# Kernel tuning notes

Hardware: AMD Instinct MI355X
Metric: run time of the kernel (lower is better)

Reference implementation:

```python
import jax, jax.numpy as jnp
from jax import lax
import numpy as np

BATCH, SEQ_LEN, ENC_IN, C_OUT = 16, 512, 32, 32
N_ORDER = 256           # window_size
MULTISCALE = (1, 2, 4)
MODES = min(32, SEQ_LEN // 2)  # = 32


def make_hippo(N, dt):
    """HiPPO-LegT transition, bilinear (Tustin) discretization, Legendre eval matrix."""
    Q = np.arange(N, dtype=np.float64)
    R = (2 * Q + 1)[:, None]
    j, i = np.meshgrid(Q, Q)
    A = np.where(i < j, -1.0, (-1.0) ** (i - j + 1)) * R
    B = (-1.0) ** Q[:, None] * R                      # [N,1]
    I = np.eye(N)
    M = I - (dt / 2.0) * A
    Ad = np.linalg.solve(M, I + (dt / 2.0) * A)
    Bd = np.linalg.solve(M, dt * B).squeeze(-1)       # [N]
    vals = np.arange(0.0, 1.0, dt)
    x = 1.0 - 2.0 * vals
    P = np.zeros((N, len(vals)))
    P[0] = 1.0
    if N > 1:
        P[1] = x
    for n in range(1, N - 1):
        P[n + 1] = ((2 * n + 1) * x * P[n] - n * P[n - 1]) / (n + 1)
    E = P.T                                           # [len(vals), N]
    return Ad.astype(np.float32), Bd.astype(np.float32), E.astype(np.float32)


def setup_inputs():
    key = jax.random.key(0)
    ks = jax.random.split(key, 12)
    inp = {}
    inp['x_enc'] = jax.random.normal(ks[0], (BATCH, SEQ_LEN, ENC_IN), jnp.float32)
    inp['x_mark_enc'] = jax.random.normal(ks[1], (BATCH, SEQ_LEN, 4), jnp.float32)
    inp['x_dec'] = jax.random.normal(ks[2], (BATCH, SEQ_LEN, ENC_IN), jnp.float32)
    inp['x_mark_dec'] = jax.random.normal(ks[3], (BATCH, SEQ_LEN, 4), jnp.float32)
    inp['affine_weight'] = jnp.ones((1, 1, ENC_IN), jnp.float32)
    inp['affine_bias'] = jnp.zeros((1, 1, ENC_IN), jnp.float32)
    scale = 1.0 / (N_ORDER * N_ORDER)
    for s in range(3):
        inp[f'wr{s}'] = scale * jax.random.uniform(ks[4 + 2 * s], (N_ORDER, N_ORDER, MODES), jnp.float32)
        inp[f'wi{s}'] = scale * jax.random.uniform(ks[5 + 2 * s], (N_ORDER, N_ORDER, MODES), jnp.float32)
    inp['mlp_w'] = 0.1 * jax.random.normal(ks[10], (1, 3), jnp.float32)
    inp['mlp_b'] = jnp.zeros((1,), jnp.float32)
    inp['proj_w'] = 0.02 * jax.random.normal(ks[11], (ENC_IN, C_OUT), jnp.float32)
    inp['proj_b'] = jnp.zeros((C_OUT,), jnp.float32)
    for s, m in enumerate(MULTISCALE):
        A, Bv, E = make_hippo(N_ORDER, 1.0 / SEQ_LEN / m)
        inp[f'A{s}'] = jnp.asarray(A)
        inp[f'Bv{s}'] = jnp.asarray(Bv)
        inp[f'E{s}'] = jnp.asarray(E)
    return inp


def _hippo_scan(x, A, Bv):
    # x: [B, L, C] -> cs: [L, B, C, N]; c_t = A c_{t-1} + B f_t (applied on last dim)
    B_, L, C = x.shape
    c0 = jnp.zeros((B_, C, A.shape[0]), x.dtype)
    At = A.T
    def step(c, f):                      # f: [B, C]
        c = c @ At + f[..., None] * Bv
        return c, c
    _, cs = lax.scan(step, c0, jnp.transpose(x, (1, 0, 2)))
    return cs


def _spectral_conv(xc, wr, wi):
    # xc: [B, C, N, L]; keep first MODES rfft bins, complex channel mix over N, irfft
    L = xc.shape[-1]
    xf = jnp.fft.rfft(xc)                                # [B,C,N,L//2+1] complex64
    W = (wr + 1j * wi).astype(jnp.complex64)             # [N,N,MODES]
    out = jnp.einsum('bjix,iox->bjox', xf[..., :MODES], W)
    out_ft = jnp.pad(out, ((0, 0), (0, 0), (0, 0), (0, L // 2 + 1 - MODES)))
    return jnp.fft.irfft(out_ft, n=L)                    # [B,C,N,L]


def _forward(x_enc, affine_weight, affine_bias, specs, mlp_w, mlp_b, proj_w, proj_b, hippos):
    means = lax.stop_gradient(jnp.mean(x_enc, axis=1, keepdims=True))
    xc = x_enc - means
    stdev = lax.stop_gradient(jnp.sqrt(jnp.var(xc, axis=1, keepdims=True) + 1e-5))
    x = xc / stdev
    x = x * affine_weight + affine_bias                  # [B, L, C]
    pred_len = SEQ_LEN
    decs = []
    for (wr, wi), (A, Bv, E) in zip(specs, hippos):
        # multiscale slice x[:, -m*pred_len:] clips to full seq_len since pred_len==seq_len
        cs = _hippo_scan(x, A, Bv)                       # [L,B,C,N]
        x_in_c = jnp.transpose(cs, (1, 2, 3, 0))         # [B,C,N,L]
        out1 = _spectral_conv(x_in_c, wr, wi)            # [B,C,N,L]
        x_dec_c = out1[..., pred_len - 1]                # [B,C,N]
        dec = x_dec_c @ E[-pred_len:, :].T               # [B,C,pred_len]
        decs.append(dec)
    stacked = jnp.stack(decs, axis=-1)                   # [B,C,P,3]
    y = stacked @ mlp_w[0] + mlp_b[0]                    # Linear(3,1) + squeeze -> [B,C,P]
    y = jnp.transpose(y, (0, 2, 1))                      # [B,P,C]
    y = (y - affine_bias) / (affine_weight + 1e-10)
    y = y * stdev + means
    return y @ proj_w + proj_b                           # OutputBlock: per-step channel projection


def reference(x_enc, x_mark_enc, x_dec, x_mark_dec, affine_weight, affine_bias,
              wr0, wi0, wr1, wi1, wr2, wi2, mlp_w, mlp_b, proj_w, proj_b,
              A0, Bv0, E0, A1, Bv1, E1, A2, Bv2, E2):
    specs = [(wr0, wi0), (wr1, wi1), (wr2, wi2)]
    hippos = [(A0, Bv0, E0), (A1, Bv1, E1), (A2, Bv2, E2)]
    return _forward(x_enc, affine_weight, affine_bias, specs, mlp_w, mlp_b, proj_w, proj_b, hippos)
```

## Files before the change

### kernel.cpp

```cpp
#include <hip/hip_runtime.h>
#include <math.h>

#define SEQ 512
#define NORD 256
#define MODES 32
#define KBIG (NORD*MODES*2)
#define PI_F 3.14159265358979323846f

typedef _Float16 half8 __attribute__((ext_vector_type(8)));
typedef float floatx4 __attribute__((ext_vector_type(4)));


struct GJob {
  const float* A; const float* B; float* C; const float* scale_ptr;
  int M, N, lda, k0, k1, atomic;
};
struct GJobs { GJob j[6]; };

__global__ __launch_bounds__(256) void gemm32_k(GJobs P) {
  GJob jb = P.j[blockIdx.z];
  int col0 = blockIdx.x * 32;
  int row0 = blockIdx.y * 32;
  if (row0 >= jb.M || col0 >= jb.N) return;
  __shared__ float As[64][34];
  __shared__ float Bs[64][36];
  int tid = threadIdx.x;
  int tx = tid & 15, ty = tid >> 4;
  const float* A = jb.A; const float* B = jb.B;
  int M = jb.M, N = jb.N, lda = jb.lda;
  int kcA = (tid & 15) * 4, rA = tid >> 4;
  int ccB = (tid & 7) * 4, kkB = tid >> 3;
  int gr0 = row0 + rA, gr1 = row0 + rA + 16;
  const float4 z4 = make_float4(0.f, 0.f, 0.f, 0.f);
  float4 a0, a1, b0, b1;
  {
    int kb = jb.k0;
    a0 = (gr0 < M) ? *(const float4*)&A[(size_t)gr0 * lda + kb + kcA] : z4;
    a1 = (gr1 < M) ? *(const float4*)&A[(size_t)gr1 * lda + kb + kcA] : z4;
    b0 = *(const float4*)&B[(size_t)(kb + kkB) * N + col0 + ccB];
    b1 = *(const float4*)&B[(size_t)(kb + kkB + 32) * N + col0 + ccB];
  }
  float acc00 = 0.f, acc01 = 0.f, acc10 = 0.f, acc11 = 0.f;
  for (int kb = jb.k0; kb < jb.k1; kb += 64) {
    As[kcA+0][rA] = a0.x; As[kcA+1][rA] = a0.y; As[kcA+2][rA] = a0.z; As[kcA+3][rA] = a0.w;
    As[kcA+0][rA+16] = a1.x; As[kcA+1][rA+16] = a1.y; As[kcA+2][rA+16] = a1.z; As[kcA+3][rA+16] = a1.w;
    *(float4*)&Bs[kkB][ccB] = b0;
    *(float4*)&Bs[kkB+32][ccB] = b1;
    __syncthreads();
    if (kb + 64 < jb.k1) {
      int kn = kb + 64;
      a0 = (gr0 < M) ? *(const float4*)&A[(size_t)gr0 * lda + kn + kcA] : z4;
      a1 = (gr1 < M) ? *(const float4*)&A[(size_t)gr1 * lda + kn + kcA] : z4;
      b0 = *(const float4*)&B[(size_t)(kn + kkB) * N + col0 + ccB];
      b1 = *(const float4*)&B[(size_t)(kn + kkB + 32) * N + col0 + ccB];
    }
    #pragma unroll
    for (int k = 0; k < 64; k++) {
      float2 av = *(float2*)&As[k][ty * 2];
      float2 bv = *(float2*)&Bs[k][tx * 2];
      acc00 += av.x * bv.x; acc01 += av.x * bv.y;
      acc10 += av.y * bv.x; acc11 += av.y * bv.y;
    }
    __syncthreads();
  }
  float sc = jb.scale_ptr ? *jb.scale_ptr : 1.f;
  int gr = row0 + ty * 2, gc = col0 + tx * 2;
  float v00 = acc00 * sc, v01 = acc01 * sc, v10 = acc10 * sc, v11 = acc11 * sc;
  if (jb.atomic) {
    if (gr < M)     { atomicAdd(&jb.C[(size_t)gr * N + gc], v00);     atomicAdd(&jb.C[(size_t)gr * N + gc + 1], v01); }
    if (gr + 1 < M) { atomicAdd(&jb.C[(size_t)(gr+1) * N + gc], v10); atomicAdd(&jb.C[(size_t)(gr+1) * N + gc + 1], v11); }
  } else {
    if (gr < M)     { jb.C[(size_t)gr * N + gc] = v00;     jb.C[(size_t)gr * N + gc + 1] = v01; }
    if (gr + 1 < M) { jb.C[(size_t)(gr+1) * N + gc] = v10; jb.C[(size_t)(gr+1) * N + gc + 1] = v11; }
  }
}


__global__ __launch_bounds__(256) void prep_k(const float* A0, const float* A1, const float* A2,
                                              const float* B0, const float* B1, const float* B2,
                                              const float* E0, const float* E1, const float* E2,
                                              float* R, float* Kry, float* Et, float* Z) {
  long bid = blockIdx.x;
  if (bid < 768) {
    long idx = bid * 256 + threadIdx.x;
    int scl = (int)(idx >> 16);
    int r = (int)(idx & 65535);
    int m = r >> 8, i2 = r & 255;
    const float* A = scl == 0 ? A0 : (scl == 1 ? A1 : A2);
    R[(size_t)scl * 2 * 65536 + (size_t)m * 256 + i2] = A[(size_t)i2 * 256 + m];
  } else if (bid < 2304) {
    long idx = (bid - 768) * 256 + threadIdx.x;
    int scl = (int)(idx / 131072);
    int r = (int)(idx % 131072);
    int p = r >> 8, o = r & 255;
    const float* E; int rows;
    if (scl == 0) { E = E0; rows = 512; }
    else if (scl == 1) { E = E1; rows = 1024; }
    else { E = E2; rows = 2048; }
    int base = rows - 512;
    Et[(size_t)scl * 131072 + (size_t)o * 512 + p] = E[(size_t)(base + p) * 256 + o];
  } else if (bid < 2307) {
    int scl = (int)(bid - 2304);
    const float* B = scl == 0 ? B0 : (scl == 1 ? B1 : B2);
    Kry[(size_t)scl * 512 * 256 + threadIdx.x] = B[threadIdx.x];
  } else {
    long idx = (bid - 2307) * 256 + threadIdx.x;
    if (idx < 655360) Z[idx] = 0.f;
  }
}


__global__ __launch_bounds__(256) void revin_k(const float* __restrict__ x,
                                               const float* __restrict__ aw,
                                               const float* __restrict__ ab,
                                               float* __restrict__ F,
                                               float* __restrict__ stats) {
  int row = blockIdx.x;
  int b = row >> 5, c = row & 31;
  int tid = threadIdx.x;
  const float* xp = x + (size_t)b * SEQ * 32 + c;
  float v0 = xp[(size_t)tid * 32];
  float v1 = xp[(size_t)(tid + 256) * 32];
  float s = v0 + v1, s2 = v0 * v0 + v1 * v1;
  for (int off = 32; off; off >>= 1) {
    s  += __shfl_down(s,  off, 64);
    s2 += __shfl_down(s2, off, 64);
  }
  __shared__ float ws1[4], ws2[4];
  __shared__ float mean_s, istd_s;
  int wid = tid >> 6, lane = tid & 63;
  if (lane == 0) { ws1[wid] = s; ws2[wid] = s2; }
  __syncthreads();
  if (tid == 0) {
    float t1 = ws1[0] + ws1[1] + ws1[2] + ws1[3];
    float t2 = ws2[0] + ws2[1] + ws2[2] + ws2[3];
    float mean = t1 / 512.f;
    float var = t2 / 512.f - mean * mean;
    float sd = sqrtf(var + 1e-5f);
    mean_s = mean; istd_s = 1.f / sd;
    stats[row] = mean; stats[512 + row] = sd;
  }
  __syncthreads();
  float w = aw[c], bb = ab[c];
  float m = mean_s, is = istd_s;
  F[(size_t)row * SEQ + tid]       = (v0 - m) * is * w + bb;
  F[(size_t)row * SEQ + tid + 256] = (v1 - m) * is * w + bb;
}


__global__ __launch_bounds__(256) void qbuildA_k(const float* __restrict__ Kry,
                                                 float2* __restrict__ Pp, int s0) {
  int bg = blockIdx.x;
  int s = s0 + (bg >> 8);
  int r = bg & 255;
  int k = r & 31, c = r >> 5;
  const float* Kry_s = Kry + (size_t)s * 131072;
  float2* P = Pp + (size_t)s * 65536;
  int i = threadIdx.x;
  float ar = 0.f, ai = 0.f;
  const float step = 2.f * PI_F / 512.f;
  int m0 = c * 64;
  for (int mm = 0; mm < 64; mm++) {
    int m = m0 + mm;
    float kap = Kry_s[(size_t)m * 256 + i];
    float sn, cn; __sincosf(step * (float)((k * m) & 511), &sn, &cn);
    ar += kap * cn; ai -= kap * sn;
  }
  P[(size_t)(c * 32 + k) * 256 + i] = make_float2(ar, ai);
}

__global__ __launch_bounds__(256) void qbuildB_k(const float* __restrict__ Kry,
                                                 const float2* __restrict__ Pp,
                                                 _Float16* __restrict__ Qf, int s0) {
  int bg = blockIdx.x;
  int slab = bg >> 8;
  int s = s0 + slab;
  int r = bg & 255;
  int ig = r & 31, c = r >> 5;
  const float* Kry_s = Kry + (size_t)s * 131072;
  const float2* P = Pp + (size_t)s * 65536;
  unsigned int* Qd = (unsigned int*)(Qf + (size_t)slab * 8388608);
  int tid = threadIdx.x;
  int k = tid & 31, il = tid >> 5;
  int i = ig * 8 + il;
  __shared__ __align__(16) unsigned int buf[16 * 256];
  float ar = 0.f, ai = 0.f;
  for (int cp = 0; cp < c; cp++) {
    float2 p = P[(size_t)(cp * 32 + k) * 256 + i];
    ar += p.x; ai += p.y;
  }
  const float step = 2.f * PI_F / 512.f;
  int m0 = c * 64;
  for (int mb = 0; mb < 64; mb += 16) {
    #pragma unroll
    for (int mm = 0; mm < 16; mm++) {
      int m = m0 + mb + mm;
      float kap = Kry_s[(size_t)m * 256 + i];
      float sn, cn; __sincosf(step * (float)((k * m) & 511), &sn, &cn);
      ar += kap * cn; ai -= kap * sn;
      int st = 511 - m;
      float sn2, cn2; __sincosf(step * (float)((k * st) & 511), &sn2, &cn2);
      float qr = ar * cn2 + ai * sn2;
      float qi = ai * cn2 - ar * sn2;
      qr = fminf(fmaxf(qr, -60000.f), 60000.f);
      qi = fminf(fmaxf(qi, -60000.f), 60000.f);
      _Float16 h0 = (_Float16)qr, h1 = (_Float16)qi;
      unsigned short u0, u1;
      __builtin_memcpy(&u0, &h0, 2); __builtin_memcpy(&u1, &h1, 2);
      buf[(st & 15) * 256 + il * 32 + k] = (unsigned int)u0 | ((unsigned int)u1 << 16);
    }
    __syncthreads();
    int st_hi = 511 - (m0 + mb);
    #pragma unroll
    for (int p = 0; p < 4; p++) {
      int idx = p * 256 + tid;
      int rr = idx >> 6, part = idx & 63;
      int st = st_hi - 15 + rr;
      uint4 v = *(uint4*)&buf[(st & 15) * 256 + part * 4];
      *(uint4*)&Qd[(size_t)st * 8192 + (size_t)ig * 256 + part * 4] = v;
    }
    __syncthreads();
  }
}


__global__ __launch_bounds__(256) void wbigT_k(const float* wr0, const float* wi0,
                                               const float* wr1, const float* wi1,
                                               const float* wr2, const float* wi2,
                                               _Float16* __restrict__ Wt, int s0) {
  int bg = blockIdx.x;
  int slab = bg >> 8;
  int s = s0 + slab;
  int r = bg & 255;
  int og = r & 31, iq = r >> 5;
  const float* wr = s == 0 ? wr0 : (s == 1 ? wr1 : wr2);
  const float* wi = s == 0 ? wi0 : (s == 1 ? wi1 : wi2);
  unsigned int* Wd = (unsigned int*)(Wt + (size_t)slab * 4194304);
  int tid = threadIdx.x;
  int ol = tid >> 5, k = tid & 31;
  int o = og * 8 + ol;
  float sn, cn; __sincosf((2.f * PI_F / 512.f) * (float)k, &sn, &cn);
  float g = ((k == 0) ? (1.f / 512.f) : (2.f / 512.f)) * 4096.f;
  float gc = g * cn, gs = g * sn;
  for (int ii = 0; ii < 32; ii++) {
    int i = iq * 32 + ii;
    float a = wr[(size_t)i * 8192 + o * 32 + k];
    float b = wi[(size_t)i * 8192 + o * 32 + k];
    float v0 = gc * a + gs * b;
    float v1 = gs * a - gc * b;
    _Float16 h0 = (_Float16)v0, h1 = (_Float16)v1;
    unsigned short u0, u1;
    __builtin_memcpy(&u0, &h0, 2); __builtin_memcpy(&u1, &h1, 2);
    Wd[(size_t)o * 8192 + (size_t)i * 32 + k] = (unsigned int)u0 | ((unsigned int)u1 << 16);
  }
}


__global__ __launch_bounds__(256) void umfma_k(const _Float16* __restrict__ Qf,
                                               const _Float16* __restrict__ Wt,
                                               float* __restrict__ U, int s0) {
  __shared__ __align__(16) _Float16 Al[8192];
  __shared__ __align__(16) _Float16 Bl[8192];
  int slab = blockIdx.z >> 4;
  int kslab = blockIdx.z & 15;
  int s = s0 + slab;
  const _Float16* Q = Qf + (size_t)slab * 8388608;
  const _Float16* W = Wt + (size_t)slab * 4194304;
  float* Us = U + (size_t)s * 131072;
  int m0 = blockIdx.x * 128;
  int n0 = blockIdx.y * 128;
  int kb0 = kslab * 1024;
  int tid = threadIdx.x;
  int w = tid >> 6, lane = tid & 63;
  int quad = lane >> 4, lm = lane & 15;
  floatx4 acc[4][4];
  #pragma unroll
  for (int a = 0; a < 4; a++)
    #pragma unroll
    for (int b = 0; b < 4; b++) acc[a][b] = (floatx4)(0.f);
  int wm = (w & 1) * 64, wn = (w >> 1) * 64;
  for (int kb = kb0; kb < kb0 + 1024; kb += 64) {
    __syncthreads();
    #pragma unroll
    for (int p = 0; p < 4; p++) {
      int idx = p * 256 + tid;
      int row = idx >> 3, kc = idx & 7;
      int slot = ((kc >> 2) * 8 + (row >> 4)) * 64 + (kc & 3) * 16 + (row & 15);
      *(half8*)&Al[slot * 8] = *(const half8*)&Q[(size_t)(m0 + row) * 16384 + kb + kc * 8];
      *(half8*)&Bl[slot * 8] = *(const half8*)&W[(size_t)(n0 + row) * 16384 + kb + kc * 8];
    }
    __syncthreads();
    #pragma unroll
    for (int ks = 0; ks < 2; ks++) {
      half8 af[4], bf[4];
      #pragma unroll
      for (int t = 0; t < 4; t++) {
        int mt = (wm >> 4) + t;
        af[t] = *(half8*)&Al[((ks * 8 + mt) * 64 + quad * 16 + lm) * 8];
        int nt = (wn >> 4) + t;
        bf[t] = *(half8*)&Bl[((ks * 8 + nt) * 64 + quad * 16 + lm) * 8];
      }
      #pragma unroll
      for (int mi = 0; mi < 4; mi++)
        #pragma unroll
        for (int ni = 0; ni < 4; ni++)
          acc[mi][ni] = __builtin_amdgcn_mfma_f32_16x16x32_f16(af[mi], bf[ni], acc[mi][ni], 0, 0, 0);
    }
  }
  #pragma unroll
  for (int mi = 0; mi < 4; mi++) {
    int gr0 = m0 + wm + mi * 16 + quad * 4;
    #pragma unroll
    for (int ni = 0; ni < 4; ni++) {
      int gc = n0 + wn + ni * 16 + lm;
      #pragma unroll
      for (int r = 0; r < 4; r++)
        atomicAdd(&Us[(size_t)(gr0 + r) * 256 + gc], acc[mi][ni][r] * (1.f / 4096.f));
    }
  }
}


__global__ __launch_bounds__(256) void final_k(const float* __restrict__ y0,
                                               const float* __restrict__ stats,
                                               const float* __restrict__ aw,
                                               const float* __restrict__ ab,
                                               const float* __restrict__ mlp_b,
                                               const float* __restrict__ pw,
                                               const float* __restrict__ pb,
                                               float* __restrict__ out) {
  int b = blockIdx.y;
  int p0 = blockIdx.x * 8;
  int tid = threadIdx.x;
  __shared__ float ys[32 * 8];
  __shared__ float pws[32 * 32];
  for (int t = tid; t < 1024; t += 256) pws[t] = pw[t];
  int c = tid >> 3, pl = tid & 7;
  int row = b * 32 + c;
  float mean = stats[row], sd = stats[512 + row];
  float raw = y0[(size_t)row * 512 + p0 + pl];
  float v = ((raw + mlp_b[0]) - ab[c]) / (aw[c] + 1e-10f) * sd + mean;
  ys[c * 8 + pl] = v;
  __syncthreads();
  int co = tid & 31; int pl2 = tid >> 5;
  float accv = pb[co];
  #pragma unroll
  for (int cc = 0; cc < 32; cc++) accv += ys[cc * 8 + pl2] * pws[cc * 32 + co];
  out[(size_t)b * 512 * 32 + (size_t)(p0 + pl2) * 32 + co] = accv;
}


extern "C" void kernel_launch(void* const* d_in, const int* in_sizes, int n_in,
                              void* d_out, int out_size, void* d_ws, size_t ws_size,
                              hipStream_t stream) {
  const float* x_enc = (const float*)d_in[0];
  const float* aw = (const float*)d_in[4];
  const float* ab = (const float*)d_in[5];
  const float* wr[3] = {(const float*)d_in[6], (const float*)d_in[8], (const float*)d_in[10]};
  const float* wi[3] = {(const float*)d_in[7], (const float*)d_in[9], (const float*)d_in[11]};
  const float* mlp_w = (const float*)d_in[12];
  const float* mlp_b = (const float*)d_in[13];
  const float* proj_w = (const float*)d_in[14];
  const float* proj_b = (const float*)d_in[15];
  const float* Am[3]  = {(const float*)d_in[16], (const float*)d_in[19], (const float*)d_in[22]};
  const float* Bv[3]  = {(const float*)d_in[17], (const float*)d_in[20], (const float*)d_in[23]};
  const float* Em[3]  = {(const float*)d_in[18], (const float*)d_in[21], (const float*)d_in[24]};

  float* w = (float*)d_ws;
  float* F     = w; w += 512 * 512;
  float* stats = w; w += 1024;
  float* Kry   = w; w += 3 * 512 * 256;
  float* R     = w; w += 3 * 2 * 65536;
  float* U     = w; w += 3 * 512 * 256;
  float* Ttot  = w; w += 512 * 512;
  float* Et    = w; w += 3 * 256 * 512;
  float* y0    = w; w += 512 * 512;
  float* Pp    = w; w += 3 * 65536 * 2;
  _Float16* Qf = (_Float16*)w;

  size_t base_bytes = (size_t)((char*)Qf - (char*)d_ws);
  size_t slab_bytes = (size_t)(8388608 + 4194304) * 2;
  int nS = (ws_size >= base_bytes + 3 * slab_bytes) ? 3 : 1;
  _Float16* Wb = Qf + (size_t)nS * 8388608;

  revin_k<<<512, 256, 0, stream>>>(x_enc, aw, ab, F, stats);
  prep_k<<<4867, 256, 0, stream>>>(Am[0], Am[1], Am[2], Bv[0], Bv[1], Bv[2],
                                   Em[0], Em[1], Em[2], R, Kry, Et, U);

  for (int j = 0; j < 9; j++) {
    GJobs P{};
    int M = 1 << j;
    int cur = j & 1;
    int nz = 0;
    for (int s = 0; s < 3; s++) {
      float* Ks = Kry + (size_t)s * 131072;
      float* Rj = R + (size_t)s * 131072 + (size_t)cur * 65536;
      float* Rn = R + (size_t)s * 131072 + (size_t)(1 - cur) * 65536;
      P.j[nz++] = {Ks, Rj, Ks + (size_t)M * 256, nullptr, M, 256, 256, 0, 256, 0};
      if (j < 8) P.j[nz++] = {Rj, Rj, Rn, nullptr, 256, 256, 256, 0, 256, 0};
    }
    gemm32_k<<<dim3(8, 8, nz), 256, 0, stream>>>(P);
  }

  if (nS == 3) {
    qbuildA_k<<<768, 256, 0, stream>>>(Kry, (float2*)Pp, 0);
    qbuildB_k<<<768, 256, 0, stream>>>(Kry, (const float2*)Pp, Qf, 0);
    wbigT_k<<<768, 256, 0, stream>>>(wr[0], wi[0], wr[1], wi[1], wr[2], wi[2], Wb, 0);
    umfma_k<<<dim3(4, 2, 48), 256, 0, stream>>>(Qf, Wb, U, 0);
  } else {
    for (int s = 0; s < 3; s++) {
      qbuildA_k<<<256, 256, 0, stream>>>(Kry, (float2*)Pp, s);
      qbuildB_k<<<256, 256, 0, stream>>>(Kry, (const float2*)Pp, Qf, s);
      wbigT_k<<<256, 256, 0, stream>>>(wr[0], wi[0], wr[1], wi[1], wr[2], wi[2], Wb, s);
      umfma_k<<<dim3(4, 2, 16), 256, 0, stream>>>(Qf, Wb, U, s);
    }
  }

  {
    GJobs P{};
    for (int s = 0; s < 3; s++)
      P.j[s] = {U + (size_t)s * 131072, Et + (size_t)s * 131072, Ttot,
                mlp_w + s, 512, 512, 256, 0, 256, 1};
    gemm32_k<<<dim3(16, 16, 3), 256, 0, stream>>>(P);
  }

  {
    GJobs P{};
    P.j[0] = {F, Ttot, y0, nullptr, 512, 512, 512, 0, 512, 0};
    gemm32_k<<<dim3(16, 16, 1), 256, 0, stream>>>(P);
  }

  final_k<<<dim3(64, 16), 256, 0, stream>>>(y0, stats, aw, ab, mlp_b, proj_w, proj_b,
                                            (float*)d_out);
}
```

Baseline: 373.2 us.

## Fuse setup kernels, overlap W-transform with Krylov GEMMs, retile MFMA operand layout

```diff
diff --git a/kernel.cpp b/kernel.cpp
--- a/kernel.cpp
+++ b/kernel.cpp
@@ -9,16 +9,54 @@
 
 typedef _Float16 half8 __attribute__((ext_vector_type(8)));
 typedef float floatx4 __attribute__((ext_vector_type(4)));
+typedef unsigned int uint;
+
 
 
 struct GJob {
   const float* A; const float* B; float* C; const float* scale_ptr;
   int M, N, lda, k0, k1, atomic;
 };
-struct GJobs { GJob j[6]; };
+struct GJobs {
+  GJob j[6];
+  const float* wwr[3]; const float* wwi[3];
+  _Float16* Wt; int nGemm; int wb_i0; int wb_slab0;
+};
 
 __global__ __launch_bounds__(256) void gemm32_k(GJobs P) {
-  GJob jb = P.j[blockIdx.z];
+  int z = blockIdx.z;
+  if (z >= P.nGemm) {
+    if (blockIdx.y != 0) return;
+    int ig = P.wb_i0 + (z - P.nGemm);
+    int s = ig >> 8, i = ig & 255;
+    const float* wr = P.wwr[s];
+    const float* wi = P.wwi[s];
+    uint* Wd = (uint*)(P.Wt + (size_t)(s - P.wb_slab0) * 4194304);
+    int j = blockIdx.x * 256 + threadIdx.x;
+    int ot = j >> 7, loc = j & 127;
+    int ks = loc >> 6, kg8 = (loc >> 4) & 3, on = loc & 15;
+    int o = ot * 16 + on, k0 = ks * 16 + kg8 * 4;
+    float4 wr4 = *(const float4*)&wr[(size_t)i * 8192 + o * 32 + k0];
+    float4 wi4 = *(const float4*)&wi[(size_t)i * 8192 + o * 32 + k0];
+    float wa[4] = {wr4.x, wr4.y, wr4.z, wr4.w};
+    float wb[4] = {wi4.x, wi4.y, wi4.z, wi4.w};
+    uint out[4];
+    #pragma unroll
+    for (int q = 0; q < 4; q++) {
+      int k = k0 + q;
+      float sn, cn; __sincosf((2.f * PI_F / 512.f) * (float)k, &sn, &cn);
+      float g = ((k == 0) ? (1.f / 512.f) : (2.f / 512.f)) * 4096.f;
+      float v0 = g * (cn * wa[q] + sn * wb[q]);
+      float v1 = g * (sn * wa[q] - cn * wb[q]);
+      _Float16 h0 = (_Float16)v0, h1 = (_Float16)v1;
+      unsigned short u0, u1;
+      __builtin_memcpy(&u0, &h0, 2); __builtin_memcpy(&u1, &h1, 2);
+      out[q] = (uint)u0 | ((uint)u1 << 16);
+    }
+    *(uint4*)&Wd[((size_t)(i * 16 + ot)) * 512 + loc * 4] = *(uint4*)out;
+    return;
+  }
+  GJob jb = P.j[z];
   int col0 = blockIdx.x * 32;
   int row0 = blockIdx.y * 32;
   if (row0 >= jb.M || col0 >= jb.N) return;
@@ -76,20 +114,23 @@
 }
 
 
-__global__ __launch_bounds__(256) void prep_k(const float* A0, const float* A1, const float* A2,
-                                              const float* B0, const float* B1, const float* B2,
-                                              const float* E0, const float* E1, const float* E2,
-                                              float* R, float* Kry, float* Et, float* Z) {
+__global__ __launch_bounds__(256) void setup_k(const float* A0, const float* A1, const float* A2,
+                                               const float* B0, const float* B1, const float* B2,
+                                               const float* E0, const float* E1, const float* E2,
+                                               const float* x, const float* aw, const float* ab,
+                                               float* R, float* Kry, float* Et, float* Z,
+                                               float* F, float* stats) {
   long bid = blockIdx.x;
+  int tid = threadIdx.x;
   if (bid < 768) {
-    long idx = bid * 256 + threadIdx.x;
+    long idx = bid * 256 + tid;
     int scl = (int)(idx >> 16);
     int r = (int)(idx & 65535);
     int m = r >> 8, i2 = r & 255;
     const float* A = scl == 0 ? A0 : (scl == 1 ? A1 : A2);
     R[(size_t)scl * 2 * 65536 + (size_t)m * 256 + i2] = A[(size_t)i2 * 256 + m];
   } else if (bid < 2304) {
-    long idx = (bid - 768) * 256 + threadIdx.x;
+    long idx = (bid - 768) * 256 + tid;
     int scl = (int)(idx / 131072);
     int r = (int)(idx % 131072);
     int p = r >> 8, o = r & 255;
@@ -102,49 +143,41 @@
   } else if (bid < 2307) {
     int scl = (int)(bid - 2304);
     const float* B = scl == 0 ? B0 : (scl == 1 ? B1 : B2);
-    Kry[(size_t)scl * 512 * 256 + threadIdx.x] = B[threadIdx.x];
+    Kry[(size_t)scl * 131072 + tid] = B[tid];
+  } else if (bid < 4867) {
+    long idx = (bid - 2307) * 256 + tid;
+    if (idx < 655360) Z[idx] = 0.f;
   } else {
-    long idx = (bid - 2307) * 256 + threadIdx.x;
-    if (idx < 655360) Z[idx] = 0.f;
-  }
-}
-
-
-__global__ __launch_bounds__(256) void revin_k(const float* __restrict__ x,
-                                               const float* __restrict__ aw,
-                                               const float* __restrict__ ab,
-                                               float* __restrict__ F,
-                                               float* __restrict__ stats) {
-  int row = blockIdx.x;
-  int b = row >> 5, c = row & 31;
-  int tid = threadIdx.x;
-  const float* xp = x + (size_t)b * SEQ * 32 + c;
-  float v0 = xp[(size_t)tid * 32];
-  float v1 = xp[(size_t)(tid + 256) * 32];
-  float s = v0 + v1, s2 = v0 * v0 + v1 * v1;
-  for (int off = 32; off; off >>= 1) {
-    s  += __shfl_down(s,  off, 64);
-    s2 += __shfl_down(s2, off, 64);
-  }
-  __shared__ float ws1[4], ws2[4];
-  __shared__ float mean_s, istd_s;
-  int wid = tid >> 6, lane = tid & 63;
-  if (lane == 0) { ws1[wid] = s; ws2[wid] = s2; }
-  __syncthreads();
-  if (tid == 0) {
-    float t1 = ws1[0] + ws1[1] + ws1[2] + ws1[3];
-    float t2 = ws2[0] + ws2[1] + ws2[2] + ws2[3];
-    float mean = t1 / 512.f;
-    float var = t2 / 512.f - mean * mean;
-    float sd = sqrtf(var + 1e-5f);
-    mean_s = mean; istd_s = 1.f / sd;
-    stats[row] = mean; stats[512 + row] = sd;
-  }
-  __syncthreads();
-  float w = aw[c], bb = ab[c];
-  float m = mean_s, is = istd_s;
-  F[(size_t)row * SEQ + tid]       = (v0 - m) * is * w + bb;
-  F[(size_t)row * SEQ + tid + 256] = (v1 - m) * is * w + bb;
+    int row = (int)(bid - 4867);
+    int b = row >> 5, c = row & 31;
+    const float* xp = x + (size_t)b * SEQ * 32 + c;
+    float v0 = xp[(size_t)tid * 32];
+    float v1 = xp[(size_t)(tid + 256) * 32];
+    float s = v0 + v1, s2 = v0 * v0 + v1 * v1;
+    for (int off = 32; off; off >>= 1) {
+      s  += __shfl_down(s,  off, 64);
+      s2 += __shfl_down(s2, off, 64);
+    }
+    __shared__ float ws1[4], ws2[4];
+    __shared__ float mean_s, istd_s;
+    int wid = tid >> 6, lane = tid & 63;
+    if (lane == 0) { ws1[wid] = s; ws2[wid] = s2; }
+    __syncthreads();
+    if (tid == 0) {
+      float t1 = ws1[0] + ws1[1] + ws1[2] + ws1[3];
+      float t2 = ws2[0] + ws2[1] + ws2[2] + ws2[3];
+      float mean = t1 / 512.f;
+      float var = t2 / 512.f - mean * mean;
+      float sd = sqrtf(var + 1e-5f);
+      mean_s = mean; istd_s = 1.f / sd;
+      stats[row] = mean; stats[512 + row] = sd;
+    }
+    __syncthreads();
+    float w = aw[c], bb = ab[c];
+    float m = mean_s, is = istd_s;
+    F[(size_t)row * SEQ + tid]       = (v0 - m) * is * w + bb;
+    F[(size_t)row * SEQ + tid + 256] = (v1 - m) * is * w + bb;
+  }
 }
 
 
@@ -169,6 +202,7 @@
   P[(size_t)(c * 32 + k) * 256 + i] = make_float2(ar, ai);
 }
 
+
 __global__ __launch_bounds__(256) void qbuildB_k(const float* __restrict__ Kry,
                                                  const float2* __restrict__ Pp,
                                                  _Float16* __restrict__ Qf, int s0) {
@@ -179,11 +213,11 @@
   int ig = r & 31, c = r >> 5;
   const float* Kry_s = Kry + (size_t)s * 131072;
   const float2* P = Pp + (size_t)s * 65536;
-  unsigned int* Qd = (unsigned int*)(Qf + (size_t)slab * 8388608);
+  uint* Qd = (uint*)(Qf + (size_t)slab * 8388608);
   int tid = threadIdx.x;
   int k = tid & 31, il = tid >> 5;
   int i = ig * 8 + il;
-  __shared__ __align__(16) unsigned int buf[16 * 256];
+  __shared__ __align__(16) uint buf[16 * 260];
   float ar = 0.f, ai = 0.f;
   for (int cp = 0; cp < c; cp++) {
     float2 p = P[(size_t)(cp * 32 + k) * 256 + i];
@@ -191,6 +225,7 @@
   }
   const float step = 2.f * PI_F / 512.f;
   int m0 = c * 64;
+  int u = tid & 31, myil = tid >> 5;
   for (int mb = 0; mb < 64; mb += 16) {
     #pragma unroll
     for (int mm = 0; mm < 16; mm++) {
@@ -207,51 +242,20 @@
       _Float16 h0 = (_Float16)qr, h1 = (_Float16)qi;
       unsigned short u0, u1;
       __builtin_memcpy(&u0, &h0, 2); __builtin_memcpy(&u1, &h1, 2);
-      buf[(st & 15) * 256 + il * 32 + k] = (unsigned int)u0 | ((unsigned int)u1 << 16);
-    }
-    __syncthreads();
-    int st_hi = 511 - (m0 + mb);
-    #pragma unroll
-    for (int p = 0; p < 4; p++) {
-      int idx = p * 256 + tid;
-      int rr = idx >> 6, part = idx & 63;
-      int st = st_hi - 15 + rr;
-      uint4 v = *(uint4*)&buf[(st & 15) * 256 + part * 4];
-      *(uint4*)&Qd[(size_t)st * 8192 + (size_t)ig * 256 + part * 4] = v;
-    }
-    __syncthreads();
-  }
-}
-
-
-__global__ __launch_bounds__(256) void wbigT_k(const float* wr0, const float* wi0,
-                                               const float* wr1, const float* wi1,
-                                               const float* wr2, const float* wi2,
-                                               _Float16* __restrict__ Wt, int s0) {
-  int bg = blockIdx.x;
-  int slab = bg >> 8;
-  int s = s0 + slab;
-  int r = bg & 255;
-  int og = r & 31, iq = r >> 5;
-  const float* wr = s == 0 ? wr0 : (s == 1 ? wr1 : wr2);
-  const float* wi = s == 0 ? wi0 : (s == 1 ? wi1 : wi2);
-  unsigned int* Wd = (unsigned int*)(Wt + (size_t)slab * 4194304);
-  int tid = threadIdx.x;
-  int ol = tid >> 5, k = tid & 31;
-  int o = og * 8 + ol;
-  float sn, cn; __sincosf((2.f * PI_F / 512.f) * (float)k, &sn, &cn);
-  float g = ((k == 0) ? (1.f / 512.f) : (2.f / 512.f)) * 4096.f;
-  float gc = g * cn, gs = g * sn;
-  for (int ii = 0; ii < 32; ii++) {
-    int i = iq * 32 + ii;
-    float a = wr[(size_t)i * 8192 + o * 32 + k];
-    float b = wi[(size_t)i * 8192 + o * 32 + k];
-    float v0 = gc * a + gs * b;
-    float v1 = gs * a - gc * b;
-    _Float16 h0 = (_Float16)v0, h1 = (_Float16)v1;
-    unsigned short u0, u1;
-    __builtin_memcpy(&u0, &h0, 2); __builtin_memcpy(&u1, &h1, 2);
-    Wd[(size_t)o * 8192 + (size_t)i * 32 + k] = (unsigned int)u0 | ((unsigned int)u1 << 16);
+      buf[(st & 15) * 260 + il * 32 + k] = (uint)u0 | ((uint)u1 << 16);
+    }
+    __syncthreads();
+    int stt = (511 - (m0 + mb)) >> 4;
+    int kc = ig * 8 + myil;
+    uint* tile = Qd + ((size_t)(kc * 32 + stt)) * 512;
+    #pragma unroll
+    for (int r4 = 0; r4 < 4; r4++) {
+      int f = u * 4 + r4;
+      int m = f & 15, kg8 = (f >> 4) & 3, ks = f >> 6;
+      uint4 v = *(uint4*)&buf[m * 260 + myil * 32 + ks * 16 + kg8 * 4];
+      *(uint4*)&tile[f * 4] = v;
+    }
+    __syncthreads();
   }
 }
 
@@ -259,17 +263,17 @@
 __global__ __launch_bounds__(256) void umfma_k(const _Float16* __restrict__ Qf,
                                                const _Float16* __restrict__ Wt,
                                                float* __restrict__ U, int s0) {
-  __shared__ __align__(16) _Float16 Al[8192];
-  __shared__ __align__(16) _Float16 Bl[8192];
+  __shared__ __align__(16) uint Al_u[4096];
+  __shared__ __align__(16) uint Bl_u[4096];
   int slab = blockIdx.z >> 4;
   int kslab = blockIdx.z & 15;
   int s = s0 + slab;
-  const _Float16* Q = Qf + (size_t)slab * 8388608;
-  const _Float16* W = Wt + (size_t)slab * 4194304;
+  const uint* Qt = (const uint*)(Qf + (size_t)slab * 8388608);
+  const uint* Wu = (const uint*)(Wt + (size_t)slab * 4194304);
   float* Us = U + (size_t)s * 131072;
-  int m0 = blockIdx.x * 128;
-  int n0 = blockIdx.y * 128;
-  int kb0 = kslab * 1024;
+  int stt0 = blockIdx.x * 8;
+  int ot0 = blockIdx.y * 8;
+  int m0 = blockIdx.x * 128, n0 = blockIdx.y * 128;
   int tid = threadIdx.x;
   int w = tid >> 6, lane = tid & 63;
   int quad = lane >> 4, lm = lane & 15;
@@ -278,27 +282,43 @@
   for (int a = 0; a < 4; a++)
     #pragma unroll
     for (int b = 0; b < 4; b++) acc[a][b] = (floatx4)(0.f);
-  int wm = (w & 1) * 64, wn = (w >> 1) * 64;
-  for (int kb = kb0; kb < kb0 + 1024; kb += 64) {
-    __syncthreads();
-    #pragma unroll
-    for (int p = 0; p < 4; p++) {
-      int idx = p * 256 + tid;
-      int row = idx >> 3, kc = idx & 7;
-      int slot = ((kc >> 2) * 8 + (row >> 4)) * 64 + (kc & 3) * 16 + (row & 15);
-      *(half8*)&Al[slot * 8] = *(const half8*)&Q[(size_t)(m0 + row) * 16384 + kb + kc * 8];
-      *(half8*)&Bl[slot * 8] = *(const half8*)&W[(size_t)(n0 + row) * 16384 + kb + kc * 8];
-    }
-    __syncthreads();
+  int wmt = (w & 1) * 4, wnt = (w >> 1) * 4;
+  uint4 qa[4], qb[4];
+  {
+    int kc = kslab * 16;
+    const uint* qsrc = Qt + ((size_t)(kc * 32 + stt0)) * 512;
+    const uint* wsrc = Wu + ((size_t)(kc * 16 + ot0)) * 512;
+    #pragma unroll
+    for (int r = 0; r < 4; r++) {
+      qa[r] = *(const uint4*)&qsrc[(r * 256 + tid) * 4];
+      qb[r] = *(const uint4*)&wsrc[(r * 256 + tid) * 4];
+    }
+  }
+  for (int it = 0; it < 16; it++) {
+    __syncthreads();
+    #pragma unroll
+    for (int r = 0; r < 4; r++) {
+      *(uint4*)&Al_u[(r * 256 + tid) * 4] = qa[r];
+      *(uint4*)&Bl_u[(r * 256 + tid) * 4] = qb[r];
+    }
+    __syncthreads();
+    if (it < 15) {
+      int kc = kslab * 16 + it + 1;
+      const uint* qsrc = Qt + ((size_t)(kc * 32 + stt0)) * 512;
+      const uint* wsrc = Wu + ((size_t)(kc * 16 + ot0)) * 512;
+      #pragma unroll
+      for (int r = 0; r < 4; r++) {
+        qa[r] = *(const uint4*)&qsrc[(r * 256 + tid) * 4];
+        qb[r] = *(const uint4*)&wsrc[(r * 256 + tid) * 4];
+      }
+    }
     #pragma unroll
     for (int ks = 0; ks < 2; ks++) {
       half8 af[4], bf[4];
       #pragma unroll
       for (int t = 0; t < 4; t++) {
-        int mt = (wm >> 4) + t;
-        af[t] = *(half8*)&Al[((ks * 8 + mt) * 64 + quad * 16 + lm) * 8];
-        int nt = (wn >> 4) + t;
-        bf[t] = *(half8*)&Bl[((ks * 8 + nt) * 64 + quad * 16 + lm) * 8];
+        af[t] = *(half8*)((_Float16*)Al_u + ((wmt + t) * 1024 + ks * 512 + lane * 8));
+        bf[t] = *(half8*)((_Float16*)Bl_u + ((wnt + t) * 1024 + ks * 512 + lane * 8));
       }
       #pragma unroll
       for (int mi = 0; mi < 4; mi++)
@@ -309,10 +329,10 @@
   }
   #pragma unroll
   for (int mi = 0; mi < 4; mi++) {
-    int gr0 = m0 + wm + mi * 16 + quad * 4;
+    int gr0 = m0 + wmt * 16 + mi * 16 + quad * 4;
     #pragma unroll
     for (int ni = 0; ni < 4; ni++) {
-      int gc = n0 + wn + ni * 16 + lm;
+      int gc = n0 + wnt * 16 + ni * 16 + lm;
       #pragma unroll
       for (int r = 0; r < 4; r++)
         atomicAdd(&Us[(size_t)(gr0 + r) * 256 + gc], acc[mi][ni][r] * (1.f / 4096.f));
@@ -321,32 +341,79 @@
 }
 
 
-__global__ __launch_bounds__(256) void final_k(const float* __restrict__ y0,
-                                               const float* __restrict__ stats,
-                                               const float* __restrict__ aw,
-                                               const float* __restrict__ ab,
-                                               const float* __restrict__ mlp_b,
-                                               const float* __restrict__ pw,
-                                               const float* __restrict__ pb,
-                                               float* __restrict__ out) {
+__global__ __launch_bounds__(256) void y0final_k(const float* __restrict__ F,
+                                                 const float* __restrict__ Ttot,
+                                                 const float* __restrict__ stats,
+                                                 const float* __restrict__ aw,
+                                                 const float* __restrict__ ab,
+                                                 const float* __restrict__ mlp_b,
+                                                 const float* __restrict__ pw,
+                                                 const float* __restrict__ pb,
+                                                 float* __restrict__ out) {
+  __shared__ float As[64][34];
+  __shared__ float Bs[64][36];
+  __shared__ float ys[32][33];
+  __shared__ float pws[1024];
+  int bxp = blockIdx.x;
   int b = blockIdx.y;
-  int p0 = blockIdx.x * 8;
+  int row0 = b * 32, col0 = bxp * 32;
   int tid = threadIdx.x;
-  __shared__ float ys[32 * 8];
-  __shared__ float pws[32 * 32];
   for (int t = tid; t < 1024; t += 256) pws[t] = pw[t];
-  int c = tid >> 3, pl = tid & 7;
-  int row = b * 32 + c;
-  float mean = stats[row], sd = stats[512 + row];
-  float raw = y0[(size_t)row * 512 + p0 + pl];
-  float v = ((raw + mlp_b[0]) - ab[c]) / (aw[c] + 1e-10f) * sd + mean;
-  ys[c * 8 + pl] = v;
+  int tx = tid & 15, ty = tid >> 4;
+  int kcA = (tid & 15) * 4, rA = tid >> 4;
+  int ccB = (tid & 7) * 4, kkB = tid >> 3;
+  int gr0 = row0 + rA, gr1 = row0 + rA + 16;
+  float4 a0, a1, b0, b1;
+  a0 = *(const float4*)&F[(size_t)gr0 * 512 + kcA];
+  a1 = *(const float4*)&F[(size_t)gr1 * 512 + kcA];
+  b0 = *(const float4*)&Ttot[(size_t)kkB * 512 + col0 + ccB];
+  b1 = *(const float4*)&Ttot[(size_t)(kkB + 32) * 512 + col0 + ccB];
+  float acc00 = 0.f, acc01 = 0.f, acc10 = 0.f, acc11 = 0.f;
+  for (int kb = 0; kb < 512; kb += 64) {
+    As[kcA+0][rA] = a0.x; As[kcA+1][rA] = a0.y; As[kcA+2][rA] = a0.z; As[kcA+3][rA] = a0.w;
+    As[kcA+0][rA+16] = a1.x; As[kcA+1][rA+16] = a1.y; As[kcA+2][rA+16] = a1.z; As[kcA+3][rA+16] = a1.w;
+    *(float4*)&Bs[kkB][ccB] = b0;
+    *(float4*)&Bs[kkB+32][ccB] = b1;
+    __syncthreads();
+    if (kb + 64 < 512) {
+      int kn = kb + 64;
+      a0 = *(const float4*)&F[(size_t)gr0 * 512 + kn + kcA];
+      a1 = *(const float4*)&F[(size_t)gr1 * 512 + kn + kcA];
+      b0 = *(const float4*)&Ttot[(size_t)(kn + kkB) * 512 + col0 + ccB];
+      b1 = *(const float4*)&Ttot[(size_t)(kn + kkB + 32) * 512 + col0 + ccB];
+    }
+    #pragma unroll
+    for (int k = 0; k < 64; k++) {
+      float2 av = *(float2*)&As[k][ty * 2];
+      float2 bv = *(float2*)&Bs[k][tx * 2];
+      acc00 += av.x * bv.x; acc01 += av.x * bv.y;
+      acc10 += av.y * bv.x; acc11 += av.y * bv.y;
+    }
+    __syncthreads();
+  }
+  float mb0 = mlp_b[0];
+  {
+    int c0 = ty * 2, c1 = ty * 2 + 1;
+    int r0g = row0 + c0, r1g = row0 + c1;
+    float mean0 = stats[r0g], sd0 = stats[512 + r0g];
+    float mean1 = stats[r1g], sd1 = stats[512 + r1g];
+    float q0 = sd0 / (aw[c0] + 1e-10f), q1 = sd1 / (aw[c1] + 1e-10f);
+    float o0 = mean0 - (ab[c0] - mb0) * q0, o1 = mean1 - (ab[c1] - mb0) * q1;
+    ys[c0][tx * 2]     = acc00 * q0 + o0;
+    ys[c0][tx * 2 + 1] = acc01 * q0 + o0;
+    ys[c1][tx * 2]     = acc10 * q1 + o1;
+    ys[c1][tx * 2 + 1] = acc11 * q1 + o1;
+  }
   __syncthreads();
-  int co = tid & 31; int pl2 = tid >> 5;
-  float accv = pb[co];
+  int p = tid >> 3, co0 = (tid & 7) * 4;
+  float4 facc = *(const float4*)&pb[co0];
   #pragma unroll
-  for (int cc = 0; cc < 32; cc++) accv += ys[cc * 8 + pl2] * pws[cc * 32 + co];
-  out[(size_t)b * 512 * 32 + (size_t)(p0 + pl2) * 32 + co] = accv;
+  for (int cc = 0; cc < 32; cc++) {
+    float f = ys[cc][p];
+    float4 pw4 = *(float4*)&pws[cc * 32 + co0];
+    facc.x += f * pw4.x; facc.y += f * pw4.y; facc.z += f * pw4.z; facc.w += f * pw4.w;
+  }
+  *(float4*)&out[(size_t)b * 16384 + (size_t)(col0 + p) * 32 + co0] = facc;
 }
 
 
@@ -374,7 +441,6 @@
   float* U     = w; w += 3 * 512 * 256;
   float* Ttot  = w; w += 512 * 512;
   float* Et    = w; w += 3 * 256 * 512;
-  float* y0    = w; w += 512 * 512;
   float* Pp    = w; w += 3 * 65536 * 2;
   _Float16* Qf = (_Float16*)w;
 
@@ -383,10 +449,11 @@
   int nS = (ws_size >= base_bytes + 3 * slab_bytes) ? 3 : 1;
   _Float16* Wb = Qf + (size_t)nS * 8388608;
 
-  revin_k<<<512, 256, 0, stream>>>(x_enc, aw, ab, F, stats);
-  prep_k<<<4867, 256, 0, stream>>>(Am[0], Am[1], Am[2], Bv[0], Bv[1], Bv[2],
-                                   Em[0], Em[1], Em[2], R, Kry, Et, U);
-
+  setup_k<<<5379, 256, 0, stream>>>(Am[0], Am[1], Am[2], Bv[0], Bv[1], Bv[2],
+                                    Em[0], Em[1], Em[2], x_enc, aw, ab,
+                                    R, Kry, Et, U, F, stats);
+
+  int wb_done = 0;
   for (int j = 0; j < 9; j++) {
     GJobs P{};
     int M = 1 << j;
@@ -399,19 +466,32 @@
       P.j[nz++] = {Ks, Rj, Ks + (size_t)M * 256, nullptr, M, 256, 256, 0, 256, 0};
       if (j < 8) P.j[nz++] = {Rj, Rj, Rn, nullptr, 256, 256, 256, 0, 256, 0};
     }
-    gemm32_k<<<dim3(8, 8, nz), 256, 0, stream>>>(P);
+    P.nGemm = nz;
+    int wb_cnt = 0;
+    if (nS == 3) {
+      wb_cnt = (j < 8) ? 86 : (768 - 86 * 8);
+      P.wwr[0] = wr[0]; P.wwr[1] = wr[1]; P.wwr[2] = wr[2];
+      P.wwi[0] = wi[0]; P.wwi[1] = wi[1]; P.wwi[2] = wi[2];
+      P.Wt = Wb; P.wb_i0 = wb_done; P.wb_slab0 = 0;
+      wb_done += wb_cnt;
+    }
+    gemm32_k<<<dim3(8, 8, nz + wb_cnt), 256, 0, stream>>>(P);
   }
 
   if (nS == 3) {
     qbuildA_k<<<768, 256, 0, stream>>>(Kry, (float2*)Pp, 0);
     qbuildB_k<<<768, 256, 0, stream>>>(Kry, (const float2*)Pp, Qf, 0);
-    wbigT_k<<<768, 256, 0, stream>>>(wr[0], wi[0], wr[1], wi[1], wr[2], wi[2], Wb, 0);
     umfma_k<<<dim3(4, 2, 48), 256, 0, stream>>>(Qf, Wb, U, 0);
   } else {
     for (int s = 0; s < 3; s++) {
+      GJobs P{};
+      P.nGemm = 0;
+      P.wwr[0] = wr[0]; P.wwr[1] = wr[1]; P.wwr[2] = wr[2];
+      P.wwi[0] = wi[0]; P.wwi[1] = wi[1]; P.wwi[2] = wi[2];
+      P.Wt = Wb; P.wb_i0 = s * 256; P.wb_slab0 = s;
+      gemm32_k<<<dim3(8, 1, 256), 256, 0, stream>>>(P);
       qbuildA_k<<<256, 256, 0, stream>>>(Kry, (float2*)Pp, s);
       qbuildB_k<<<256, 256, 0, stream>>>(Kry, (const float2*)Pp, Qf, s);
-      wbigT_k<<<256, 256, 0, stream>>>(wr[0], wi[0], wr[1], wi[1], wr[2], wi[2], Wb, s);
       umfma_k<<<dim3(4, 2, 16), 256, 0, stream>>>(Qf, Wb, U, s);
     }
   }
@@ -421,15 +501,10 @@
     for (int s = 0; s < 3; s++)
       P.j[s] = {U + (size_t)s * 131072, Et + (size_t)s * 131072, Ttot,
                 mlp_w + s, 512, 512, 256, 0, 256, 1};
+    P.nGemm = 3;
     gemm32_k<<<dim3(16, 16, 3), 256, 0, stream>>>(P);
   }
 
-  {
-    GJobs P{};
-    P.j[0] = {F, Ttot, y0, nullptr, 512, 512, 512, 0, 512, 0};
-    gemm32_k<<<dim3(16, 16, 1), 256, 0, stream>>>(P);
-  }
-
-  final_k<<<dim3(64, 16), 256, 0, stream>>>(y0, stats, aw, ab, mlp_b, proj_w, proj_b,
-                                            (float*)d_out);
-}
+  y0final_k<<<dim3(16, 16), 256, 0, stream>>>(F, Ttot, stats, aw, ab, mlp_b,
+                                              proj_w, proj_b, (float*)d_out);
+}
```

New measurement: 399.2 us. 7.0% more time.
